# Optimization experiments

Hardware: AMD Instinct MI355X
Metric: run time of the kernel (lower is better)

Reference implementation:

```python
import jax, jax.numpy as jnp
import numpy as np

C = 128          # inchannel
CH = C // 2      # projected channels
N_, D_, H_, W_ = 2, 16, 16, 16


def setup_inputs() -> dict:
    key = jax.random.key(0)
    kx, kq, kk, kv, kp = jax.random.split(key, 5)
    s_in = 1.0 / np.sqrt(C)
    s_mid = 1.0 / np.sqrt(CH)
    return {
        "x": jax.random.normal(kx, (N_, C, D_, H_, W_), dtype=jnp.float32),
        "Wq": jax.random.normal(kq, (CH, C), dtype=jnp.float32) * s_in,
        "Wk": jax.random.normal(kk, (CH, C), dtype=jnp.float32) * s_in,
        "Wv": jax.random.normal(kv, (CH, C), dtype=jnp.float32) * s_in,
        "Wpost": jax.random.normal(kp, (C, CH), dtype=jnp.float32) * s_mid,
    }


def reference(x, Wq, Wk, Wv, Wpost):
    n, c_in, d, h, w = x.shape
    npos = d * h * w
    xf = x.reshape(n, c_in, npos)                     # (n, C, N)
    # 1x1x1 conv3d (no bias) == channel-mixing matmul
    q = jnp.einsum('oc,ncx->nox', Wq, xf)             # (n, CH, N)
    k = jnp.einsum('oc,ncx->nox', Wk, xf)             # (n, CH, N)
    v = jnp.einsum('oc,ncx->nox', Wv, xf)             # (n, CH, N)
    # atten_map[b,i,j] = sum_c k[b,c,i] * q[b,c,j], softmax over j (dim=2)
    scores = jnp.einsum('nci,ncj->nij', k, q)         # (n, N, N)
    attn = jax.nn.softmax(scores, axis=2)
    # val @ attn: out[b,c,j] = sum_i v[b,c,i] * attn[b,i,j]
    agg = jnp.einsum('nci,nij->ncj', v, attn)         # (n, CH, N)
    post = jnp.einsum('oc,ncx->nox', Wpost, agg)      # (n, C, N)
    return post.reshape(n, c_in, d, h, w) + x
```

## Files before the change

kernel.cpp:

```cpp
#include <hip/hip_runtime.h>
#include <math.h>

#define NB   2
#define CIN  128
#define CH   64
#define NPOS 4096

typedef __attribute__((ext_vector_type(8))) short s16x8;
typedef __attribute__((ext_vector_type(4))) float f32x4;

__device__ __forceinline__ unsigned int bfrne(float f) {
    unsigned int u = __float_as_uint(f);
    return (u + 0x7FFFu + ((u >> 16) & 1u)) >> 16;
}
__device__ __forceinline__ unsigned int pk_rne(float lo, float hi) {
    return bfrne(lo) | (bfrne(hi) << 16);
}
__device__ __forceinline__ unsigned int pk_fast(float lo, float hi) {
    unsigned int a = (__float_as_uint(lo) + 0x8000u) >> 16;
    unsigned int b = (__float_as_uint(hi) + 0x8000u) & 0xFFFF0000u;
    return a | b;
}
__device__ __forceinline__ float bf2f(unsigned short h) {
    return __uint_as_float(((unsigned int)h) << 16);
}

__global__ __launch_bounds__(256) void packw_kernel(
    const float* __restrict__ Wq, const float* __restrict__ Wk,
    const float* __restrict__ Wv, const float* __restrict__ Wpost,
    unsigned short* __restrict__ Wb)
{
    const int gid = blockIdx.x * 256 + threadIdx.x;
    const int base = gid * 4;
    const int mat = base >> 13, off = base & 8191;
    const float* src = (mat == 0) ? Wq : (mat == 1) ? Wk : (mat == 2) ? Wv : Wpost;
    float4 f = *(const float4*)&src[off];
    uint2 st = make_uint2(pk_rne(f.x, f.y), pk_rne(f.z, f.w));
    *(uint2*)&Wb[mat * 8192 + off] = st;
}

#define XTS 132
__global__ __launch_bounds__(256) void qkv_kernel(
    const float* __restrict__ x, const unsigned short* __restrict__ Wb,
    unsigned short* __restrict__ kT, unsigned short* __restrict__ qT,
    unsigned short* __restrict__ vbs)
{
    __shared__ __align__(16) float xT[16 * XTS];
    const int b  = blockIdx.y;
    const int p0 = blockIdx.x * 16;
    const int tid = threadIdx.x;

    #pragma unroll
    for (int it = 0; it < 2; ++it) {
        int idx = it * 256 + tid;
        int c = idx >> 2, p4 = (idx & 3) * 4;
        float4 g = *(const float4*)&x[((size_t)b * CIN + c) * NPOS + p0 + p4];
        xT[(p4 + 0) * XTS + c] = g.x;
        xT[(p4 + 1) * XTS + c] = g.y;
        xT[(p4 + 2) * XTS + c] = g.z;
        xT[(p4 + 3) * XTS + c] = g.w;
    }
    __syncthreads();

    const int w = tid >> 6, l = tid & 63, lm = l & 15, lq = l >> 4;
    const int p = p0 + lm;

    s16x8 Bhi[4], Blo[4];
    #pragma unroll
    for (int ck = 0; ck < 4; ++ck) {
        const float* xr = &xT[lm * XTS + ck * 32 + lq * 8];
        union { unsigned int u[4]; s16x8 v; } chv, clv;
        #pragma unroll
        for (int j = 0; j < 4; ++j) {
            float x0 = xr[2 * j], x1 = xr[2 * j + 1];
            unsigned int h0 = bfrne(x0), h1 = bfrne(x1);
            chv.u[j] = h0 | (h1 << 16);
            clv.u[j] = pk_rne(x0 - __uint_as_float(h0 << 16),
                              x1 - __uint_as_float(h1 << 16));
        }
        Bhi[ck] = chv.v; Blo[ck] = clv.v;
    }

    #pragma unroll
    for (int t3 = 0; t3 < 3; ++t3) {
        const int tile = w * 3 + t3;
        const int mat = tile >> 2, o0 = (tile & 3) * 16;
        const unsigned short* Wm = Wb + mat * 8192;
        f32x4 acc = {0.f, 0.f, 0.f, 0.f};
        #pragma unroll
        for (int ck = 0; ck < 4; ++ck) {
            s16x8 aW = *(const s16x8*)&Wm[(o0 + lm) * CIN + ck * 32 + lq * 8];
            acc = __builtin_amdgcn_mfma_f32_16x16x32_bf16(aW, Bhi[ck], acc, 0,0,0);
            acc = __builtin_amdgcn_mfma_f32_16x16x32_bf16(aW, Blo[ck], acc, 0,0,0);
        }
        if (mat < 2) {
            unsigned short* dst = (mat == 0) ? qT : kT;
            uint2 st = make_uint2(pk_rne(acc[0], acc[1]), pk_rne(acc[2], acc[3]));
            *(uint2*)&dst[((size_t)b * NPOS + p) * CH + o0 + lq * 4] = st;
        } else {
            #pragma unroll
            for (int r = 0; r < 4; ++r)
                vbs[((size_t)b * CH + o0 + lq * 4 + r) * NPOS + p] =
                    (unsigned short)bfrne(acc[r]);
        }
    }
}

__global__ __launch_bounds__(256, 4) void stats_kernel(
    const unsigned short* __restrict__ kT,
    const unsigned short* __restrict__ qT,
    float* __restrict__ lpart)
{
    __shared__ __align__(16) unsigned short qbuf[2][4096];
    const int b  = blockIdx.z;
    const int jq = blockIdx.y;
    const int i0 = blockIdx.x * 64;
    const int tid = threadIdx.x;
    const int w = tid >> 6, l = tid & 63, lm = l & 15, lq = l >> 4;

    s16x8 a0 = *(const s16x8*)&kT[
        ((size_t)b * NPOS + i0 + w * 16 + lm) * CH + lq * 8];
    s16x8 a1 = *(const s16x8*)&kT[
        ((size_t)b * NPOS + i0 + w * 16 + lm) * CH + 32 + lq * 8];

    const unsigned short* qpt =
        qT + ((size_t)b * NPOS + jq * 512 + w * 16 + lm) * CH + lq * 8;
    s16x8 st0 = *(const s16x8*)(qpt);
    s16x8 st1 = *(const s16x8*)(qpt + 32);

    float rs[4] = {0.f, 0.f, 0.f, 0.f};
    for (int t = 0; t < 8; ++t) {
        const int buf = t & 1;
        *(s16x8*)&qbuf[buf][(2 * w + 0) * 512 + l * 8] = st0;
        *(s16x8*)&qbuf[buf][(2 * w + 1) * 512 + l * 8] = st1;
        if (t < 7) {
            const unsigned short* qn = qpt + (size_t)(t + 1) * 64 * CH;
            st0 = *(const s16x8*)(qn);
            st1 = *(const s16x8*)(qn + 32);
        }
        __syncthreads();
        #pragma unroll
        for (int js = 0; js < 4; ++js) {
            s16x8 b0 = *(const s16x8*)&qbuf[buf][(js * 2 + 0) * 512 + l * 8];
            s16x8 b1 = *(const s16x8*)&qbuf[buf][(js * 2 + 1) * 512 + l * 8];
            f32x4 sc = {0.f, 0.f, 0.f, 0.f};
            sc = __builtin_amdgcn_mfma_f32_16x16x32_bf16(a0, b0, sc, 0,0,0);
            sc = __builtin_amdgcn_mfma_f32_16x16x32_bf16(a1, b1, sc, 0,0,0);
            rs[0] += __expf(sc[0]); rs[1] += __expf(sc[1]);
            rs[2] += __expf(sc[2]); rs[3] += __expf(sc[3]);
        }
    }

    #pragma unroll
    for (int r = 0; r < 4; ++r) {
        rs[r] += __shfl_xor(rs[r], 1);
        rs[r] += __shfl_xor(rs[r], 2);
        rs[r] += __shfl_xor(rs[r], 4);
        rs[r] += __shfl_xor(rs[r], 8);
    }
    if (lm == 0) {
        #pragma unroll
        for (int r = 0; r < 4; ++r)
            lpart[(size_t)jq * NB * NPOS + b * NPOS
                  + i0 + w * 16 + lq * 4 + r] = rs[r];
    }
}

__global__ __launch_bounds__(256) void gl_kernel(
    const float* __restrict__ lpart, float* __restrict__ gl)
{
    const int idx4 = blockIdx.x * 256 + threadIdx.x;
    const int base = idx4 * 4;
    float sx = 0.f, sy = 0.f, sz = 0.f, sw = 0.f;
    #pragma unroll
    for (int qq = 0; qq < 8; ++qq) {
        float4 lv = *(const float4*)(lpart + (size_t)qq * NB * NPOS + base);
        sx += lv.x; sy += lv.y; sz += lv.z; sw += lv.w;
    }
    float4 o = make_float4(1.f / sx, 1.f / sy, 1.f / sz, 1.f / sw);
    *(float4*)&gl[base] = o;
}

__global__ __launch_bounds__(256, 4) void agg_kernel(
    const unsigned short* __restrict__ kT,
    const unsigned short* __restrict__ qT,
    const unsigned short* __restrict__ vbs,
    const float* __restrict__ gl,
    unsigned short* __restrict__ U)
{
    __shared__ __align__(16) unsigned short kbuf[2][2048];
    __shared__ __align__(16) unsigned short vbuf[2][2048];
    __shared__ __align__(16) float rls[512];
    const int b  = blockIdx.z;
    const int iq = blockIdx.y;
    const int j0 = blockIdx.x * 128;
    const int tid = threadIdx.x;
    const int w = tid >> 6, l = tid & 63, lm = l & 15, lq = l >> 4;

    *(float2*)&rls[tid * 2] =
        *(const float2*)&gl[(size_t)b * NPOS + iq * 512 + tid * 2];

    s16x8 qb[2][2];
    #pragma unroll
    for (int js = 0; js < 2; ++js)
        #pragma unroll
        for (int kc = 0; kc < 2; ++kc)
            qb[js][kc] = *(const s16x8*)&qT[
                ((size_t)b * NPOS + j0 + w * 32 + js * 16 + lm) * CH + kc * 32 + lq * 8];

    int addr[4];
    #pragma unroll
    for (int d = 0; d < 4; ++d)
        addr[d] = (lm + 16 * (2 * (lq & 1) + (d >> 1))) << 2;
    const bool lowhalf = (lq < 2);

    const unsigned short* kpt = kT
        + ((size_t)b * NPOS + iq * 512 + (w >> 1) * 16 + lm) * CH
        + (w & 1) * 32 + lq * 8;
    const unsigned short* vpt = vbs
        + ((size_t)b * CH + w * 16 + lm) * NPOS + iq * 512 + lq * 8;

    f32x4 acc[2][4] = {};
    s16x8 kst = *(const s16x8*)kpt;
    s16x8 vst = *(const s16x8*)vpt;

    for (int t = 0; t < 16; ++t) {
        const int buf = t & 1;
        *(s16x8*)&kbuf[buf][w * 512 + l * 8] = kst;
        *(s16x8*)&vbuf[buf][w * 512 + l * 8] = vst;
        if (t < 15) {
            kst = *(const s16x8*)(kpt + (t + 1) * 32 * CH);
            vst = *(const s16x8*)(vpt + (t + 1) * 32);
        }
        __syncthreads();

        s16x8 kA[2][2], vA[4];
        #pragma unroll
        for (int s = 0; s < 2; ++s)
            #pragma unroll
            for (int kc = 0; kc < 2; ++kc)
                kA[s][kc] = *(const s16x8*)&kbuf[buf][(s * 2 + kc) * 512 + l * 8];
        #pragma unroll
        for (int cs = 0; cs < 4; ++cs)
            vA[cs] = *(const s16x8*)&vbuf[buf][cs * 512 + l * 8];

        f32x4 rl0 = *(const f32x4*)&rls[t * 32 + lq * 4];
        f32x4 rl1 = *(const f32x4*)&rls[t * 32 + 16 + lq * 4];

        #pragma unroll
        for (int js = 0; js < 2; ++js) {
            f32x4 s0 = {0,0,0,0}, s1 = {0,0,0,0};
            s0 = __builtin_amdgcn_mfma_f32_16x16x32_bf16(kA[0][0], qb[js][0], s0, 0,0,0);
            s0 = __builtin_amdgcn_mfma_f32_16x16x32_bf16(kA[0][1], qb[js][1], s0, 0,0,0);
            s1 = __builtin_amdgcn_mfma_f32_16x16x32_bf16(kA[1][0], qb[js][0], s1, 0,0,0);
            s1 = __builtin_amdgcn_mfma_f32_16x16x32_bf16(kA[1][1], qb[js][1], s1, 0,0,0);

            unsigned int P0[2], P1[2];
            P0[0] = pk_fast(__expf(s0[0]) * rl0[0], __expf(s0[1]) * rl0[1]);
            P0[1] = pk_fast(__expf(s0[2]) * rl0[2], __expf(s0[3]) * rl0[3]);
            P1[0] = pk_fast(__expf(s1[0]) * rl1[0], __expf(s1[1]) * rl1[1]);
            P1[1] = pk_fast(__expf(s1[2]) * rl1[2], __expf(s1[3]) * rl1[3]);

            union { unsigned int u[4]; s16x8 v; } B;
            #pragma unroll
            for (int d = 0; d < 4; ++d) {
                int t0 = __builtin_amdgcn_ds_bpermute(addr[d], (int)P0[d & 1]);
                int t1 = __builtin_amdgcn_ds_bpermute(addr[d], (int)P1[d & 1]);
                B.u[d] = lowhalf ? (unsigned int)t0 : (unsigned int)t1;
            }
            #pragma unroll
            for (int cs = 0; cs < 4; ++cs)
                acc[js][cs] = __builtin_amdgcn_mfma_f32_16x16x32_bf16(
                    vA[cs], B.v, acc[js][cs], 0,0,0);
        }
    }

    unsigned short* Up = U + ((size_t)iq * NB + b) * NPOS * CH;
    #pragma unroll
    for (int js = 0; js < 2; ++js)
        #pragma unroll
        for (int cs = 0; cs < 4; ++cs) {
            uint2 st = make_uint2(pk_rne(acc[js][cs][0], acc[js][cs][1]),
                                  pk_rne(acc[js][cs][2], acc[js][cs][3]));
            *(uint2*)&Up[(size_t)(j0 + w * 32 + js * 16 + lm) * CH
                         + cs * 16 + lq * 4] = st;
        }
}

__global__ __launch_bounds__(256) void post_kernel(
    const float* __restrict__ x, const unsigned short* __restrict__ Wb,
    const unsigned short* __restrict__ U, float* __restrict__ out)
{
    const int b  = blockIdx.y;
    const int p0 = blockIdx.x * 32;
    const int tid = threadIdx.x;
    const int w = tid >> 6, l = tid & 63, lm = l & 15, lq = l >> 4;
    const int psub = (w & 1) * 16, ohalf = w >> 1;
    const int p = p0 + psub + lm;
    const size_t PS = (size_t)NB * NPOS * CH;

    const unsigned short* u = U + ((size_t)b * NPOS + p) * CH;
    const unsigned short* Wpb = Wb + 3 * 8192;
    s16x8 Bf[2];
    #pragma unroll
    for (int ck = 0; ck < 2; ++ck) {
        float sv[8] = {};
        #pragma unroll
        for (int qq = 0; qq < 8; ++qq) {
            union { s16x8 v; unsigned short us[8]; } uu;
            uu.v = *(const s16x8*)(u + (size_t)qq * PS + ck * 32 + lq * 8);
            #pragma unroll
            for (int j = 0; j < 8; ++j) sv[j] += bf2f(uu.us[j]);
        }
        union { unsigned int u[4]; s16x8 v; } cb;
        #pragma unroll
        for (int j = 0; j < 4; ++j) cb.u[j] = pk_rne(sv[2*j], sv[2*j+1]);
        Bf[ck] = cb.v;
    }

    #pragma unroll
    for (int ot = 0; ot < 4; ++ot) {
        const int o0 = (ohalf * 4 + ot) * 16;
        f32x4 acc = {0.f, 0.f, 0.f, 0.f};
        #pragma unroll
        for (int ck = 0; ck < 2; ++ck) {
            s16x8 aW = *(const s16x8*)&Wpb[(o0 + lm) * CH + ck * 32 + lq * 8];
            acc = __builtin_amdgcn_mfma_f32_16x16x32_bf16(aW, Bf[ck], acc, 0,0,0);
        }
        #pragma unroll
        for (int r = 0; r < 4; ++r) {
            size_t gi = ((size_t)b * CIN + o0 + lq * 4 + r) * NPOS + p;
            out[gi] = x[gi] + acc[r];
        }
    }
}

extern "C" void kernel_launch(void* const* d_in, const int* in_sizes, int n_in,
                              void* d_out, int out_size, void* d_ws, size_t ws_size,
                              hipStream_t stream) {
    const float* x     = (const float*)d_in[0];
    const float* Wq    = (const float*)d_in[1];
    const float* Wk    = (const float*)d_in[2];
    const float* Wv    = (const float*)d_in[3];
    const float* Wpost = (const float*)d_in[4];
    float* out = (float*)d_out;

    unsigned short* kT  = (unsigned short*)d_ws;
    unsigned short* qT  = kT + (size_t)NB * NPOS * CH;
    unsigned short* vbs = qT + (size_t)NB * NPOS * CH;
    unsigned short* Wb  = vbs + (size_t)NB * NPOS * CH;
    float* lpart = (float*)(Wb + 4 * 8192);
    float* gl    = lpart + (size_t)8 * NB * NPOS;
    unsigned short* U = (unsigned short*)(gl + (size_t)NB * NPOS);

    packw_kernel<<<dim3(32), 256, 0, stream>>>(Wq, Wk, Wv, Wpost, Wb);
    qkv_kernel  <<<dim3(NPOS / 16, NB), 256, 0, stream>>>(x, Wb, kT, qT, vbs);
    stats_kernel<<<dim3(NPOS / 64, 8, NB), 256, 0, stream>>>(kT, qT, lpart);
    gl_kernel   <<<dim3(8), 256, 0, stream>>>(lpart, gl);
    agg_kernel  <<<dim3(NPOS / 128, 8, NB), 256, 0, stream>>>(kT, qT, vbs, gl, U);
    post_kernel <<<dim3(NPOS / 32, NB), 256, 0, stream>>>(x, Wb, U, out);
}
```

Before: 107.7 us.

## Drop weight-pack and reduce kernels, fuse conversions, enlarge stats tile, use LDS transpose

Removes the separate weight packing kernel by converting fp32 weights to bf16 inline in the qkv and post kernels. Removes the gl reduction kernel by summing the partial row sums and taking reciprocals at the start of agg_kernel. Doubles the rows per stats block so each staged q tile feeds twice as many MFMAs. Replaces the ds_bpermute register shuffle in agg with an LDS write and read. The goal is fewer launches and less shuffle overhead, at the cost of redundant weight conversion and redundant lpart summing in every block.

```diff
diff --git a/kernel.cpp b/kernel.cpp
--- a/kernel.cpp
+++ b/kernel.cpp
@@ -25,23 +25,11 @@
     return __uint_as_float(((unsigned int)h) << 16);
 }
 
-__global__ __launch_bounds__(256) void packw_kernel(
-    const float* __restrict__ Wq, const float* __restrict__ Wk,
-    const float* __restrict__ Wv, const float* __restrict__ Wpost,
-    unsigned short* __restrict__ Wb)
-{
-    const int gid = blockIdx.x * 256 + threadIdx.x;
-    const int base = gid * 4;
-    const int mat = base >> 13, off = base & 8191;
-    const float* src = (mat == 0) ? Wq : (mat == 1) ? Wk : (mat == 2) ? Wv : Wpost;
-    float4 f = *(const float4*)&src[off];
-    uint2 st = make_uint2(pk_rne(f.x, f.y), pk_rne(f.z, f.w));
-    *(uint2*)&Wb[mat * 8192 + off] = st;
-}
-
 #define XTS 132
 __global__ __launch_bounds__(256) void qkv_kernel(
-    const float* __restrict__ x, const unsigned short* __restrict__ Wb,
+    const float* __restrict__ x,
+    const float* __restrict__ Wq, const float* __restrict__ Wk,
+    const float* __restrict__ Wv,
     unsigned short* __restrict__ kT, unsigned short* __restrict__ qT,
     unsigned short* __restrict__ vbs)
 {
@@ -85,13 +73,16 @@
     for (int t3 = 0; t3 < 3; ++t3) {
         const int tile = w * 3 + t3;
         const int mat = tile >> 2, o0 = (tile & 3) * 16;
-        const unsigned short* Wm = Wb + mat * 8192;
+        const float* __restrict__ W = (mat == 0) ? Wq : (mat == 1) ? Wk : Wv;
         f32x4 acc = {0.f, 0.f, 0.f, 0.f};
         #pragma unroll
         for (int ck = 0; ck < 4; ++ck) {
-            s16x8 aW = *(const s16x8*)&Wm[(o0 + lm) * CIN + ck * 32 + lq * 8];
-            acc = __builtin_amdgcn_mfma_f32_16x16x32_bf16(aW, Bhi[ck], acc, 0,0,0);
-            acc = __builtin_amdgcn_mfma_f32_16x16x32_bf16(aW, Blo[ck], acc, 0,0,0);
+            const float* wp = W + (o0 + lm) * CIN + ck * 32 + lq * 8;
+            union { unsigned int u[4]; s16x8 v; } ca;
+            #pragma unroll
+            for (int j = 0; j < 4; ++j) ca.u[j] = pk_rne(wp[2*j], wp[2*j+1]);
+            acc = __builtin_amdgcn_mfma_f32_16x16x32_bf16(ca.v, Bhi[ck], acc, 0,0,0);
+            acc = __builtin_amdgcn_mfma_f32_16x16x32_bf16(ca.v, Blo[ck], acc, 0,0,0);
         }
         if (mat < 2) {
             unsigned short* dst = (mat == 0) ? qT : kT;
@@ -114,21 +105,24 @@
     __shared__ __align__(16) unsigned short qbuf[2][4096];
     const int b  = blockIdx.z;
     const int jq = blockIdx.y;
-    const int i0 = blockIdx.x * 64;
+    const int i0 = blockIdx.x * 128;
     const int tid = threadIdx.x;
     const int w = tid >> 6, l = tid & 63, lm = l & 15, lq = l >> 4;
 
-    s16x8 a0 = *(const s16x8*)&kT[
-        ((size_t)b * NPOS + i0 + w * 16 + lm) * CH + lq * 8];
-    s16x8 a1 = *(const s16x8*)&kT[
-        ((size_t)b * NPOS + i0 + w * 16 + lm) * CH + 32 + lq * 8];
+    s16x8 a[2][2];
+    #pragma unroll
+    for (int s = 0; s < 2; ++s)
+        #pragma unroll
+        for (int kc = 0; kc < 2; ++kc)
+            a[s][kc] = *(const s16x8*)&kT[
+                ((size_t)b * NPOS + i0 + w * 32 + s * 16 + lm) * CH + kc * 32 + lq * 8];
 
     const unsigned short* qpt =
         qT + ((size_t)b * NPOS + jq * 512 + w * 16 + lm) * CH + lq * 8;
     s16x8 st0 = *(const s16x8*)(qpt);
     s16x8 st1 = *(const s16x8*)(qpt + 32);
 
-    float rs[4] = {0.f, 0.f, 0.f, 0.f};
+    float rs[2][4] = {};
     for (int t = 0; t < 8; ++t) {
         const int buf = t & 1;
         *(s16x8*)&qbuf[buf][(2 * w + 0) * 512 + l * 8] = st0;
@@ -143,53 +137,46 @@
         for (int js = 0; js < 4; ++js) {
             s16x8 b0 = *(const s16x8*)&qbuf[buf][(js * 2 + 0) * 512 + l * 8];
             s16x8 b1 = *(const s16x8*)&qbuf[buf][(js * 2 + 1) * 512 + l * 8];
-            f32x4 sc = {0.f, 0.f, 0.f, 0.f};
-            sc = __builtin_amdgcn_mfma_f32_16x16x32_bf16(a0, b0, sc, 0,0,0);
-            sc = __builtin_amdgcn_mfma_f32_16x16x32_bf16(a1, b1, sc, 0,0,0);
-            rs[0] += __expf(sc[0]); rs[1] += __expf(sc[1]);
-            rs[2] += __expf(sc[2]); rs[3] += __expf(sc[3]);
-        }
-    }
-
-    #pragma unroll
-    for (int r = 0; r < 4; ++r) {
-        rs[r] += __shfl_xor(rs[r], 1);
-        rs[r] += __shfl_xor(rs[r], 2);
-        rs[r] += __shfl_xor(rs[r], 4);
-        rs[r] += __shfl_xor(rs[r], 8);
-    }
+            #pragma unroll
+            for (int s = 0; s < 2; ++s) {
+                f32x4 sc = {0.f, 0.f, 0.f, 0.f};
+                sc = __builtin_amdgcn_mfma_f32_16x16x32_bf16(a[s][0], b0, sc, 0,0,0);
+                sc = __builtin_amdgcn_mfma_f32_16x16x32_bf16(a[s][1], b1, sc, 0,0,0);
+                rs[s][0] += __expf(sc[0]); rs[s][1] += __expf(sc[1]);
+                rs[s][2] += __expf(sc[2]); rs[s][3] += __expf(sc[3]);
+            }
+        }
+    }
+
+    #pragma unroll
+    for (int s = 0; s < 2; ++s)
+        #pragma unroll
+        for (int r = 0; r < 4; ++r) {
+            rs[s][r] += __shfl_xor(rs[s][r], 1);
+            rs[s][r] += __shfl_xor(rs[s][r], 2);
+            rs[s][r] += __shfl_xor(rs[s][r], 4);
+            rs[s][r] += __shfl_xor(rs[s][r], 8);
+        }
     if (lm == 0) {
         #pragma unroll
-        for (int r = 0; r < 4; ++r)
-            lpart[(size_t)jq * NB * NPOS + b * NPOS
-                  + i0 + w * 16 + lq * 4 + r] = rs[r];
-    }
-}
-
-__global__ __launch_bounds__(256) void gl_kernel(
-    const float* __restrict__ lpart, float* __restrict__ gl)
-{
-    const int idx4 = blockIdx.x * 256 + threadIdx.x;
-    const int base = idx4 * 4;
-    float sx = 0.f, sy = 0.f, sz = 0.f, sw = 0.f;
-    #pragma unroll
-    for (int qq = 0; qq < 8; ++qq) {
-        float4 lv = *(const float4*)(lpart + (size_t)qq * NB * NPOS + base);
-        sx += lv.x; sy += lv.y; sz += lv.z; sw += lv.w;
-    }
-    float4 o = make_float4(1.f / sx, 1.f / sy, 1.f / sz, 1.f / sw);
-    *(float4*)&gl[base] = o;
+        for (int s = 0; s < 2; ++s)
+            #pragma unroll
+            for (int r = 0; r < 4; ++r)
+                lpart[(size_t)jq * NB * NPOS + b * NPOS
+                      + i0 + w * 32 + s * 16 + lq * 4 + r] = rs[s][r];
+    }
 }
 
 __global__ __launch_bounds__(256, 4) void agg_kernel(
     const unsigned short* __restrict__ kT,
     const unsigned short* __restrict__ qT,
     const unsigned short* __restrict__ vbs,
-    const float* __restrict__ gl,
+    const float* __restrict__ lpart,
     unsigned short* __restrict__ U)
 {
     __shared__ __align__(16) unsigned short kbuf[2][2048];
     __shared__ __align__(16) unsigned short vbuf[2][2048];
+    __shared__ __align__(16) unsigned short wts[4][16][40];
     __shared__ __align__(16) float rls[512];
     const int b  = blockIdx.z;
     const int iq = blockIdx.y;
@@ -197,8 +184,17 @@
     const int tid = threadIdx.x;
     const int w = tid >> 6, l = tid & 63, lm = l & 15, lq = l >> 4;
 
-    *(float2*)&rls[tid * 2] =
-        *(const float2*)&gl[(size_t)b * NPOS + iq * 512 + tid * 2];
+    {
+        const float* lp = lpart + (size_t)b * NPOS + iq * 512 + tid * 2;
+        float s0 = 0.f, s1 = 0.f;
+        #pragma unroll
+        for (int qq = 0; qq < 8; ++qq) {
+            float2 lv = *(const float2*)(lp + (size_t)qq * NB * NPOS);
+            s0 += lv.x; s1 += lv.y;
+        }
+        rls[tid * 2 + 0] = 1.0f / s0;
+        rls[tid * 2 + 1] = 1.0f / s1;
+    }
 
     s16x8 qb[2][2];
     #pragma unroll
@@ -207,12 +203,6 @@
         for (int kc = 0; kc < 2; ++kc)
             qb[js][kc] = *(const s16x8*)&qT[
                 ((size_t)b * NPOS + j0 + w * 32 + js * 16 + lm) * CH + kc * 32 + lq * 8];
-
-    int addr[4];
-    #pragma unroll
-    for (int d = 0; d < 4; ++d)
-        addr[d] = (lm + 16 * (2 * (lq & 1) + (d >> 1))) << 2;
-    const bool lowhalf = (lq < 2);
 
     const unsigned short* kpt = kT
         + ((size_t)b * NPOS + iq * 512 + (w >> 1) * 16 + lm) * CH
@@ -261,17 +251,14 @@
             P1[0] = pk_fast(__expf(s1[0]) * rl1[0], __expf(s1[1]) * rl1[1]);
             P1[1] = pk_fast(__expf(s1[2]) * rl1[2], __expf(s1[3]) * rl1[3]);
 
-            union { unsigned int u[4]; s16x8 v; } B;
-            #pragma unroll
-            for (int d = 0; d < 4; ++d) {
-                int t0 = __builtin_amdgcn_ds_bpermute(addr[d], (int)P0[d & 1]);
-                int t1 = __builtin_amdgcn_ds_bpermute(addr[d], (int)P1[d & 1]);
-                B.u[d] = lowhalf ? (unsigned int)t0 : (unsigned int)t1;
-            }
+            *(uint2*)&wts[w][lm][4 * lq]      = make_uint2(P0[0], P0[1]);
+            *(uint2*)&wts[w][lm][16 + 4 * lq] = make_uint2(P1[0], P1[1]);
+            s16x8 Bv = *(const s16x8*)&wts[w][lm][8 * lq];
+
             #pragma unroll
             for (int cs = 0; cs < 4; ++cs)
                 acc[js][cs] = __builtin_amdgcn_mfma_f32_16x16x32_bf16(
-                    vA[cs], B.v, acc[js][cs], 0,0,0);
+                    vA[cs], Bv, acc[js][cs], 0,0,0);
         }
     }
 
@@ -288,7 +275,7 @@
 }
 
 __global__ __launch_bounds__(256) void post_kernel(
-    const float* __restrict__ x, const unsigned short* __restrict__ Wb,
+    const float* __restrict__ x, const float* __restrict__ Wpost,
     const unsigned short* __restrict__ U, float* __restrict__ out)
 {
     const int b  = blockIdx.y;
@@ -300,7 +287,6 @@
     const size_t PS = (size_t)NB * NPOS * CH;
 
     const unsigned short* u = U + ((size_t)b * NPOS + p) * CH;
-    const unsigned short* Wpb = Wb + 3 * 8192;
     s16x8 Bf[2];
     #pragma unroll
     for (int ck = 0; ck < 2; ++ck) {
@@ -324,8 +310,11 @@
         f32x4 acc = {0.f, 0.f, 0.f, 0.f};
         #pragma unroll
         for (int ck = 0; ck < 2; ++ck) {
-            s16x8 aW = *(const s16x8*)&Wpb[(o0 + lm) * CH + ck * 32 + lq * 8];
-            acc = __builtin_amdgcn_mfma_f32_16x16x32_bf16(aW, Bf[ck], acc, 0,0,0);
+            const float* wp = Wpost + (o0 + lm) * CH + ck * 32 + lq * 8;
+            union { unsigned int u[4]; s16x8 v; } ca;
+            #pragma unroll
+            for (int j = 0; j < 4; ++j) ca.u[j] = pk_rne(wp[2*j], wp[2*j+1]);
+            acc = __builtin_amdgcn_mfma_f32_16x16x32_bf16(ca.v, Bf[ck], acc, 0,0,0);
         }
         #pragma unroll
         for (int r = 0; r < 4; ++r) {
@@ -348,15 +337,11 @@
     unsigned short* kT  = (unsigned short*)d_ws;
     unsigned short* qT  = kT + (size_t)NB * NPOS * CH;
     unsigned short* vbs = qT + (size_t)NB * NPOS * CH;
-    unsigned short* Wb  = vbs + (size_t)NB * NPOS * CH;
-    float* lpart = (float*)(Wb + 4 * 8192);
-    float* gl    = lpart + (size_t)8 * NB * NPOS;
-    unsigned short* U = (unsigned short*)(gl + (size_t)NB * NPOS);
-
-    packw_kernel<<<dim3(32), 256, 0, stream>>>(Wq, Wk, Wv, Wpost, Wb);
-    qkv_kernel  <<<dim3(NPOS / 16, NB), 256, 0, stream>>>(x, Wb, kT, qT, vbs);
-    stats_kernel<<<dim3(NPOS / 64, 8, NB), 256, 0, stream>>>(kT, qT, lpart);
-    gl_kernel   <<<dim3(8), 256, 0, stream>>>(lpart, gl);
-    agg_kernel  <<<dim3(NPOS / 128, 8, NB), 256, 0, stream>>>(kT, qT, vbs, gl, U);
-    post_kernel <<<dim3(NPOS / 32, NB), 256, 0, stream>>>(x, Wb, U, out);
-}
+    float* lpart = (float*)(vbs + (size_t)NB * NPOS * CH);
+    unsigned short* U = (unsigned short*)(lpart + (size_t)8 * NB * NPOS);
+
+    qkv_kernel  <<<dim3(NPOS / 16, NB),    256, 0, stream>>>(x, Wq, Wk, Wv, kT, qT, vbs);
+    stats_kernel<<<dim3(NPOS / 128, 8, NB), 256, 0, stream>>>(kT, qT, lpart);
+    agg_kernel  <<<dim3(NPOS / 128, 8, NB), 256, 0, stream>>>(kT, qT, vbs, lpart, U);
+    post_kernel <<<dim3(NPOS / 32, NB),    256, 0, stream>>>(x, Wpost, U, out);
+}
```

Result: no change. 108.1 us (+0.4%).
